# Kernel tuning notes

Measured on AMD Instinct MI355X. Metric: run time of the kernel, lower is better.

The kernel has to match this reference:

```python
import jax, jax.numpy as jnp
import numpy as np

L, B, C, N, M, H = 256, 128, 20, 30, 3, 1024  # length, batch, cond_dim, noise_dim, midi_dim, hidden
P_DROP = 0.6


def _lstm_cell(x, h, c, Wih, Whh, bih, bhh):
    # torch.nn.LSTMCell: gates ordered i, f, g, o
    gates = x @ Wih.T + h @ Whh.T + bih + bhh
    i, f, g, o = jnp.split(gates, 4, axis=-1)
    c_new = jax.nn.sigmoid(f) * c + jax.nn.sigmoid(i) * jnp.tanh(g)
    h_new = jax.nn.sigmoid(o) * jnp.tanh(c_new)
    return h_new, c_new


def setup_inputs():
    key = jax.random.key(0)
    ks = jax.random.split(key, 16)
    keep = 1.0 - P_DROP
    s = lambda k, shape: jax.random.normal(k, shape, jnp.float32) * np.float32(1.0 / np.sqrt(H))
    return {
        "condition": jax.random.normal(ks[0], (L, B, C), jnp.float32),
        "noise": jax.random.normal(ks[1], (B, N), jnp.float32),
        "h_init": jax.random.uniform(ks[2], (B, H), jnp.float32),
        "c_init": jax.random.uniform(ks[3], (B, H), jnp.float32),
        "dropout_mask": (jax.random.uniform(ks[4], (L, B, H)) < keep).astype(jnp.float32) / np.float32(keep),
        "Wih0": s(ks[5], (4 * H, C + N)), "Whh0": s(ks[6], (4 * H, H)),
        "bih0": jnp.zeros(4 * H, jnp.float32), "bhh0": jnp.zeros(4 * H, jnp.float32),
        "Wih1": s(ks[7], (4 * H, C + M)), "Whh1": s(ks[8], (4 * H, H)),
        "bih1": jnp.zeros(4 * H, jnp.float32), "bhh1": jnp.zeros(4 * H, jnp.float32),
        "Wih2": s(ks[9], (4 * H, H)), "Whh2": s(ks[10], (4 * H, H)),
        "bih2": jnp.zeros(4 * H, jnp.float32), "bhh2": jnp.zeros(4 * H, jnp.float32),
        "Wfc": s(ks[11], (M, H)), "bfc": jnp.zeros(M, jnp.float32),
    }


def reference(condition, noise, h_init, c_init, dropout_mask,
              Wih0, Whh0, bih0, bhh0, Wih1, Whh1, bih1, bhh1,
              Wih2, Whh2, bih2, bhh2, Wfc, bfc):
    # step 0: lstmcell0 on cat(condition[0], noise); h1==h2==h_init, c1==c2==c_init
    h1, c1 = _lstm_cell(jnp.concatenate([condition[0], noise], axis=1),
                        h_init, c_init, Wih0, Whh0, bih0, bhh0)
    h1 = h1 * dropout_mask[0]
    h2, c2 = _lstm_cell(h1, h_init, c_init, Wih2, Whh2, bih2, bhh2)
    out0 = h2 @ Wfc.T + bfc  # [B, M]

    def step(carry, xs):
        h1, c1, h2, c2, out = carry
        cond_t, mask_t = xs
        h1, c1 = _lstm_cell(jnp.concatenate([cond_t, out], axis=1),
                            h1, c1, Wih1, Whh1, bih1, bhh1)
        h1 = h1 * mask_t
        h2, c2 = _lstm_cell(h1, h2, c2, Wih2, Whh2, bih2, bhh2)
        out = h2 @ Wfc.T + bfc
        return (h1, c1, h2, c2, out), out

    _, outs = jax.lax.scan(step, (h1, c1, h2, c2, out0),
                           (condition[1:], dropout_mask[1:]))
    return jnp.concatenate([out0[None], outs], axis=0)  # [L, B, M]
```

## Files before the change

### kernel.cpp

```cpp
#include <hip/hip_runtime.h>
#include <math.h>

#define Bb   128
#define Hd   1024
#define Ld   256
#define Cd   20
#define Nd   30
#define Md   3

using bfrag = __attribute__((ext_vector_type(8)))  short;
using f16v  = __attribute__((ext_vector_type(16))) float;

union Pack8 { bfrag v; unsigned short u[8]; };

__device__ __forceinline__ float sigm(float x) { return 1.0f / (1.0f + expf(-x)); }

__device__ __forceinline__ unsigned short bf_rne(float x) {
    unsigned u = __float_as_uint(x);
    unsigned r = (u + 0x7fffu + ((u >> 16) & 1u)) >> 16;
    return (unsigned short)r;
}
__device__ __forceinline__ float bf_f(unsigned short h) {
    return __uint_as_float(((unsigned)h) << 16);
}

#define MFMA(a,b,c) __builtin_amdgcn_mfma_f32_32x32x16_bf16((a),(b),(c),0,0,0)

__device__ __forceinline__ void gld_lds16(const void* g, void* s) {
    __builtin_amdgcn_global_load_lds((const __attribute__((address_space(1))) void*)g,
                                     (__attribute__((address_space(3))) void*)s, 16, 0, 0);
}
#define WAIT_VM(n) __builtin_amdgcn_s_waitcnt(0x0F70 | (n))
#define BARRIER()  __builtin_amdgcn_s_barrier()

__global__ void cast_kernel(const float* __restrict__ src,
                            unsigned short* __restrict__ dst, int n)
{
    for (int i = blockIdx.x * blockDim.x + threadIdx.x; i < n; i += gridDim.x * blockDim.x)
        dst[i] = bf_rne(src[i]);
}

__global__ void cast_pad_kernel(const float* __restrict__ src,
                                unsigned short* __restrict__ dst,
                                int rows, int K, int Kp)
{
    int n = rows * Kp;
    for (int i = blockIdx.x * blockDim.x + threadIdx.x; i < n; i += gridDim.x * blockDim.x) {
        int r = i / Kp, k = i - r * Kp;
        dst[i] = bf_rne((k < K) ? src[r * K + k] : 0.0f);
    }
}

__global__ void split_kernel(const float* __restrict__ src,
                             unsigned short* __restrict__ hi,
                             unsigned short* __restrict__ lo, int n)
{
    for (int i = blockIdx.x * blockDim.x + threadIdx.x; i < n; i += gridDim.x * blockDim.x) {
        float x = src[i];
        unsigned short h = bf_rne(x);
        hi[i] = h;
        lo[i] = bf_rne(x - bf_f(h));
    }
}

template<int MODE>
__global__ __launch_bounds__(512, 1) void mfma_cell(
    const unsigned short* __restrict__ Ahi0, const unsigned short* __restrict__ Alo0,
    const unsigned short* __restrict__ W0,
    const unsigned short* __restrict__ Ahi1, const unsigned short* __restrict__ Alo1,
    const unsigned short* __restrict__ W1,
    const float* __restrict__ condt, const float* __restrict__ outprev,
    const unsigned short* __restrict__ Wsm,
    const float* __restrict__ bih, const float* __restrict__ bhh,
    const float* __restrict__ cprev, float* __restrict__ cnew,
    const float* __restrict__ maskt,
    unsigned short* __restrict__ Hhi, unsigned short* __restrict__ Hlo,
    const float* __restrict__ Wfc, const float* __restrict__ bfc,
    float* __restrict__ outp)
{
    __shared__ unsigned short Abuf[2][2][32 * 128];
    __shared__ unsigned short Wbuf[2][64 * 128];
    __shared__ float part[8][32][65];
    __shared__ float hbuf[32][16];

    const int bid   = blockIdx.x;
    const int mtile = (bid >> 3) & 3;
    const int jtile = (bid & 7) * 8 + (bid >> 5);
    const int j0 = jtile * 16;
    const int m0 = mtile * 32;

    const int tid  = threadIdx.x;
    const int wave = tid >> 6;
    const int lane = tid & 63;
    const int ml   = lane & 31;
    const int q    = lane >> 5;

    if (MODE == 1 && bid == 0) {
        for (int i = tid; i < Bb * Md; i += 512) outp[i] = bfc[i % Md];
    }

    const int g0 = ml >> 4, jj0 = ml & 15;
    const size_t row0 = (size_t)(g0 * Hd + j0 + jj0);
    const size_t row1 = (size_t)((g0 + 2) * Hd + j0 + jj0);

    f16v C0, C1;
    #pragma unroll
    for (int r = 0; r < 16; ++r) { C0[r] = 0.0f; C1[r] = 0.0f; }

    constexpr int NC = (MODE == 1) ? 8 : 16;

    auto stage = [&](int c, int p) {
        const unsigned short *Ah, *Al, *Wg; int cb;
        if (MODE == 2 && c >= 8) { Ah = Ahi1; Al = Alo1; Wg = W1; cb = (c - 8) * 128; }
        else                     { Ah = Ahi0; Al = Alo0; Wg = W0; cb = c * 128; }
        {
            const int m = tid >> 4, bp = tid & 15, bs = bp ^ (m & 15);
            const size_t goff = (size_t)(m0 + m) * Hd + cb + bs * 8;
            gld_lds16(Ah + goff, &Abuf[p][0][wave * 512]);
            gld_lds16(Al + goff, &Abuf[p][1][wave * 512]);
        }
        #pragma unroll
        for (int r = 0; r < 2; ++r) {
            const int f = r * 512 + tid;
            const int n = f >> 4, bp = f & 15, bs = bp ^ (n & 15);
            const size_t goff = (size_t)((n >> 4) * Hd + j0 + (n & 15)) * Hd + cb + bs * 8;
            gld_lds16(Wg + goff, &Wbuf[p][r * 4096 + wave * 512]);
        }
    };

    stage(0, 0);
    for (int c = 0; c < NC; ++c) {
        const int p = c & 1;
        if (c + 1 < NC) { stage(c + 1, p ^ 1); WAIT_VM(4); }
        else            { WAIT_VM(0); }
        BARRIER();
        {
            const int b = 2 * wave + q;
            const int soff = (b ^ (ml & 15)) << 3;
            bfrag ah  = *(const bfrag*)&Abuf[p][0][ml * 128 + soff];
            bfrag al  = *(const bfrag*)&Abuf[p][1][ml * 128 + soff];
            bfrag w0f = *(const bfrag*)&Wbuf[p][ml * 128 + soff];
            bfrag w1f = *(const bfrag*)&Wbuf[p][(ml + 32) * 128 + soff];
            C0 = MFMA(ah, w0f, C0);
            C1 = MFMA(ah, w1f, C1);
            C0 = MFMA(al, w0f, C0);
            C1 = MFMA(al, w1f, C1);
        }
        BARRIER();
    }

    if (MODE == 1 && wave == 0) {
        const float* crow = condt + (m0 + ml) * Cd;
        const float* orow = outprev + (m0 + ml) * Md;
        float xv[2][8];
        #pragma unroll
        for (int j = 0; j < 8; ++j) { xv[0][j] = 0.f; xv[1][j] = 0.f; }
        if (q == 0) {
            #pragma unroll
            for (int j = 0; j < 8; ++j) xv[0][j] = crow[j];
            xv[1][0] = crow[16]; xv[1][1] = crow[17];
            xv[1][2] = crow[18]; xv[1][3] = crow[19];
            xv[1][4] = orow[0];  xv[1][5] = orow[1];  xv[1][6] = orow[2];
        } else {
            #pragma unroll
            for (int j = 0; j < 8; ++j) xv[0][j] = crow[8 + j];
        }
        #pragma unroll
        for (int ch = 0; ch < 2; ++ch) {
            Pack8 ah, al;
            #pragma unroll
            for (int j = 0; j < 8; ++j) {
                unsigned short h = bf_rne(xv[ch][j]);
                ah.u[j] = h;
                al.u[j] = bf_rne(xv[ch][j] - bf_f(h));
            }
            const int kk = ch * 16 + 8 * q;
            bfrag b0 = *(const bfrag*)(Wsm + row0 * 32 + kk);
            bfrag b1 = *(const bfrag*)(Wsm + row1 * 32 + kk);
            C0 = MFMA(ah.v, b0, C0);
            C1 = MFMA(ah.v, b1, C1);
            C0 = MFMA(al.v, b0, C0);
            C1 = MFMA(al.v, b1, C1);
        }
    }

    #pragma unroll
    for (int r = 0; r < 16; ++r) {
        const int mrow = (r & 3) + 8 * (r >> 2) + 4 * q;
        part[wave][mrow][ml]      = C0[r];
        part[wave][mrow][32 + ml] = C1[r];
    }
    __syncthreads();

    {
        const int m  = tid >> 4;
        const int jj = tid & 15;
        float g[4];
        #pragma unroll
        for (int gg = 0; gg < 4; ++gg) {
            float s = 0.0f;
            #pragma unroll
            for (int w = 0; w < 8; ++w) s += part[w][m][gg * 16 + jj];
            const int n = gg * Hd + j0 + jj;
            g[gg] = s + bih[n] + bhh[n];
        }
        const int b  = m0 + m;
        const int jc = j0 + jj;
        const size_t idx = (size_t)b * Hd + jc;
        float cp = cprev[idx];
        float cn = sigm(g[1]) * cp + sigm(g[0]) * tanhf(g[2]);
        float hv = sigm(g[3]) * tanhf(cn);
        if (MODE == 1) hv *= maskt[idx];
        cnew[idx] = cn;
        unsigned short hh = bf_rne(hv);
        Hhi[idx] = hh;
        Hlo[idx] = bf_rne(hv - bf_f(hh));
        if (MODE == 2) hbuf[m][jj] = hv;
    }

    if (MODE == 2) {
        __syncthreads();
        if (tid < 32) {
            const int b = m0 + tid;
            #pragma unroll
            for (int mm = 0; mm < Md; ++mm) {
                float s = 0.0f;
                #pragma unroll
                for (int jj = 0; jj < 16; ++jj) s += hbuf[tid][jj] * Wfc[mm * Hd + j0 + jj];
                atomicAdd(&outp[b * Md + mm], s);
            }
        }
    }
}

#define BT   64
#define JT   8
#define RT   32
#define KC   64
#define NT   256
#define NCHUNK 16
#define XSs  68
#define SMs  52
#define GBs  33

__global__ __launch_bounds__(NT) void lstm_cell_kernel(
    const float* __restrict__ Xbig0, const float* __restrict__ Wbig0,
    const float* __restrict__ Xbig1, const float* __restrict__ Wbig1,
    const float* __restrict__ Xsm0p, int K0,
    const float* __restrict__ Xsm1p, int K1,
    const float* __restrict__ Wsmall,
    const float* __restrict__ bih, const float* __restrict__ bhh,
    const float* __restrict__ cprev, float* __restrict__ cnew,
    const float* __restrict__ mask,
    float* __restrict__ hnew,
    const float* __restrict__ Wfc, const float* __restrict__ bfc,
    float* __restrict__ outp, int initOut)
{
    __shared__ float Xs[BT][XSs];
    __shared__ float Ws[RT][XSs];
    __shared__ float gbuf[BT][GBs];
    __shared__ float hbuf[BT][JT];
    __shared__ float Xsm[BT][SMs];
    __shared__ float Wsm[RT][SMs];

    const int tid = threadIdx.x;
    const int j0  = blockIdx.x * JT;
    const int b0  = blockIdx.y * BT;
    const int jp  = tid & 15;
    const int bq  = tid >> 4;

    auto GROW = [&](int r) { return ((r >> 3) * Hd + j0 + (r & 7)); };

    float acc[4][2];
    #pragma unroll
    for (int i = 0; i < 4; ++i) { acc[i][0] = 0.f; acc[i][1] = 0.f; }

    if (initOut && blockIdx.x == 0 && blockIdx.y == 0) {
        for (int i = tid; i < Bb * 3; i += NT) outp[i] = bfc[i % 3];
    }

    for (int seg = 0; seg < 2; ++seg) {
        const float* __restrict__ Xg = (seg == 0) ? Xbig0 : Xbig1;
        const float* __restrict__ Wg = (seg == 0) ? Wbig0 : Wbig1;
        if (Xg == nullptr) continue;

        float4 xr[4], wr[2];
        #pragma unroll
        for (int p = 0; p < 4; ++p) {
            int fi = p * NT + tid; int bloc = fi >> 4; int kq = fi & 15;
            xr[p] = *(const float4*)(Xg + (size_t)(b0 + bloc) * Hd + kq * 4);
        }
        #pragma unroll
        for (int p = 0; p < 2; ++p) {
            int fi = p * NT + tid; int r = fi >> 4; int kq = fi & 15;
            wr[p] = *(const float4*)(Wg + (size_t)GROW(r) * Hd + kq * 4);
        }
        #pragma unroll
        for (int p = 0; p < 4; ++p) { int fi = p * NT + tid; *(float4*)&Xs[fi >> 4][(fi & 15) * 4] = xr[p]; }
        #pragma unroll
        for (int p = 0; p < 2; ++p) { int fi = p * NT + tid; *(float4*)&Ws[fi >> 4][(fi & 15) * 4] = wr[p]; }
        __syncthreads();

        for (int kc = 0; kc < NCHUNK; ++kc) {
            const bool more = (kc + 1) < NCHUNK;
            if (more) {
                const int k0n = (kc + 1) * KC;
                #pragma unroll
                for (int p = 0; p < 4; ++p) {
                    int fi = p * NT + tid; int bloc = fi >> 4; int kq = fi & 15;
                    xr[p] = *(const float4*)(Xg + (size_t)(b0 + bloc) * Hd + k0n + kq * 4);
                }
                #pragma unroll
                for (int p = 0; p < 2; ++p) {
                    int fi = p * NT + tid; int r = fi >> 4; int kq = fi & 15;
                    wr[p] = *(const float4*)(Wg + (size_t)GROW(r) * Hd + k0n + kq * 4);
                }
            }
            #pragma unroll 4
            for (int kk = 0; kk < KC; kk += 4) {
                float4 w0 = *(const float4*)&Ws[jp][kk];
                float4 w1 = *(const float4*)&Ws[jp + 16][kk];
                #pragma unroll
                for (int bb = 0; bb < 4; ++bb) {
                    float4 xvv = *(const float4*)&Xs[bq + 16 * bb][kk];
                    acc[bb][0] += xvv.x * w0.x + xvv.y * w0.y + xvv.z * w0.z + xvv.w * w0.w;
                    acc[bb][1] += xvv.x * w1.x + xvv.y * w1.y + xvv.z * w1.z + xvv.w * w1.w;
                }
            }
            __syncthreads();
            if (more) {
                #pragma unroll
                for (int p = 0; p < 4; ++p) { int fi = p * NT + tid; *(float4*)&Xs[fi >> 4][(fi & 15) * 4] = xr[p]; }
                #pragma unroll
                for (int p = 0; p < 2; ++p) { int fi = p * NT + tid; *(float4*)&Ws[fi >> 4][(fi & 15) * 4] = wr[p]; }
                __syncthreads();
            }
        }
    }

    if (Wsmall) {
        const int Kt = K0 + K1;
        for (int i = tid; i < BT * Kt; i += NT) {
            int bloc = i / Kt, k = i % Kt;
            Xsm[bloc][k] = (k < K0) ? Xsm0p[(size_t)(b0 + bloc) * K0 + k]
                                    : Xsm1p[(size_t)(b0 + bloc) * K1 + (k - K0)];
        }
        for (int i = tid; i < RT * Kt; i += NT) {
            int r = i / Kt, k = i % Kt;
            Wsm[r][k] = Wsmall[(size_t)GROW(r) * Kt + k];
        }
        __syncthreads();
        for (int k = 0; k < Kt; ++k) {
            float w0 = Wsm[jp][k], w1 = Wsm[jp + 16][k];
            #pragma unroll
            for (int bb = 0; bb < 4; ++bb) {
                float xvv = Xsm[bq + 16 * bb][k];
                acc[bb][0] += xvv * w0;
                acc[bb][1] += xvv * w1;
            }
        }
    }

    __syncthreads();
    #pragma unroll
    for (int bb = 0; bb < 4; ++bb) {
        gbuf[bq + 16 * bb][jp]      = acc[bb][0];
        gbuf[bq + 16 * bb][jp + 16] = acc[bb][1];
    }
    __syncthreads();

    for (int p = tid; p < BT * JT; p += NT) {
        int bloc = p & (BT - 1);
        int j    = p >> 6;
        int bg   = b0 + bloc;
        int jc   = j0 + j;
        float gi = gbuf[bloc][j]      + bih[jc]          + bhh[jc];
        float gf = gbuf[bloc][8 + j]  + bih[Hd + jc]     + bhh[Hd + jc];
        float gg = gbuf[bloc][16 + j] + bih[2 * Hd + jc] + bhh[2 * Hd + jc];
        float go = gbuf[bloc][24 + j] + bih[3 * Hd + jc] + bhh[3 * Hd + jc];
        float cp = cprev[(size_t)bg * Hd + jc];
        float cn = sigm(gf) * cp + sigm(gi) * tanhf(gg);
        float hv = sigm(go) * tanhf(cn);
        if (mask) hv *= mask[(size_t)bg * Hd + jc];
        cnew[(size_t)bg * Hd + jc] = cn;
        hnew[(size_t)bg * Hd + jc] = hv;
        hbuf[bloc][j] = hv;
    }

    if (Wfc) {
        __syncthreads();
        if (tid < BT) {
            int bg = b0 + tid;
            #pragma unroll
            for (int m = 0; m < 3; ++m) {
                float s = 0.f;
                #pragma unroll
                for (int j = 0; j < JT; ++j) s += hbuf[tid][j] * Wfc[m * Hd + j0 + j];
                atomicAdd(&outp[bg * 3 + m], s);
            }
        }
    }
}

extern "C" void kernel_launch(void* const* d_in, const int* in_sizes, int n_in,
                              void* d_out, int out_size, void* d_ws, size_t ws_size,
                              hipStream_t stream)
{
    (void)in_sizes; (void)n_in; (void)out_size;
    const float* cond   = (const float*)d_in[0];
    const float* noise  = (const float*)d_in[1];
    const float* h_init = (const float*)d_in[2];
    const float* c_init = (const float*)d_in[3];
    const float* dmask  = (const float*)d_in[4];
    const float* Wih0   = (const float*)d_in[5];
    const float* Whh0   = (const float*)d_in[6];
    const float* bih0   = (const float*)d_in[7];
    const float* bhh0   = (const float*)d_in[8];
    const float* Wih1   = (const float*)d_in[9];
    const float* Whh1   = (const float*)d_in[10];
    const float* bih1   = (const float*)d_in[11];
    const float* bhh1   = (const float*)d_in[12];
    const float* Wih2   = (const float*)d_in[13];
    const float* Whh2   = (const float*)d_in[14];
    const float* bih2   = (const float*)d_in[15];
    const float* bhh2   = (const float*)d_in[16];
    const float* Wfc    = (const float*)d_in[17];
    const float* bfc    = (const float*)d_in[18];
    float* out = (float*)d_out;

    char* wsb = (char*)d_ws;
    size_t off = 0;
    auto alloc = [&](size_t bytes) { size_t o = off; off += (bytes + 255) & ~(size_t)255; return o; };

    const size_t WBIG = (size_t)4 * Hd * Hd * 2;
    const size_t HB   = (size_t)Bb * Hd * 2;
    const size_t HF   = (size_t)Bb * Hd * 4;

    size_t o_w1 = alloc(WBIG);
    size_t o_w2 = alloc(WBIG);
    size_t o_w3 = alloc(WBIG);
    size_t o_wsm = alloc((size_t)4 * Hd * 32 * 2);
    size_t o_h1h[2] = { alloc(HB), alloc(HB) };
    size_t o_h1l[2] = { alloc(HB), alloc(HB) };
    size_t o_h2h[2] = { alloc(HB), alloc(HB) };
    size_t o_h2l[2] = { alloc(HB), alloc(HB) };
    size_t o_c1 = alloc(HF), o_c2 = alloc(HF);
    size_t o_f1 = alloc(HF), o_f2 = alloc(HF);
    const size_t needed = off;

    if (ws_size < needed) {
        float* ws = (float*)d_ws;
        const size_t S = (size_t)Bb * Hd;
        float* h1a = ws;         float* h1b = ws + S;
        float* h2a = ws + 2 * S; float* h2b = ws + 3 * S;
        float* c1  = ws + 4 * S; float* c2  = ws + 5 * S;
        dim3 grid(Hd / JT, Bb / BT);
        dim3 blk(NT);
        lstm_cell_kernel<<<grid, blk, 0, stream>>>(
            h_init, Whh0, nullptr, nullptr, cond, Cd, noise, Nd, Wih0,
            bih0, bhh0, c_init, c1, dmask, h1a, nullptr, bfc, out, 1);
        lstm_cell_kernel<<<grid, blk, 0, stream>>>(
            h1a, Wih2, h_init, Whh2, nullptr, 0, nullptr, 0, nullptr,
            bih2, bhh2, c_init, c2, nullptr, h2a, Wfc, bfc, out, 0);
        const float* h1prev = h1a; const float* h2prev = h2a;
        for (int t = 1; t < Ld; ++t) {
            float* h1cur = (t & 1) ? h1b : h1a;
            float* h2cur = (t & 1) ? h2b : h2a;
            lstm_cell_kernel<<<grid, blk, 0, stream>>>(
                h1prev, Whh1, nullptr, nullptr,
                cond + (size_t)t * Bb * Cd, Cd, out + (size_t)(t - 1) * Bb * Md, Md, Wih1,
                bih1, bhh1, c1, c1, dmask + (size_t)t * Bb * Hd, h1cur,
                nullptr, bfc, out + (size_t)t * Bb * Md, 1);
            lstm_cell_kernel<<<grid, blk, 0, stream>>>(
                h1cur, Wih2, h2prev, Whh2, nullptr, 0, nullptr, 0, nullptr,
                bih2, bhh2, c2, c2, nullptr, h2cur, Wfc, bfc, out + (size_t)t * Bb * Md, 0);
            h1prev = h1cur; h2prev = h2cur;
        }
        return;
    }

    auto U16 = [&](size_t o) { return (unsigned short*)(wsb + o); };
    auto F32 = [&](size_t o) { return (float*)(wsb + o); };

    const int NW = 4 * Hd * Hd;
    cast_kernel<<<2048, 256, 0, stream>>>(Whh1, U16(o_w1), NW);
    cast_kernel<<<2048, 256, 0, stream>>>(Wih2, U16(o_w2), NW);
    cast_kernel<<<2048, 256, 0, stream>>>(Whh2, U16(o_w3), NW);
    cast_pad_kernel<<<512, 256, 0, stream>>>(Wih1, U16(o_wsm), 4 * Hd, Cd + Md, 32);

    {
        dim3 grid(Hd / JT, Bb / BT);
        dim3 blk(NT);
        lstm_cell_kernel<<<grid, blk, 0, stream>>>(
            h_init, Whh0, nullptr, nullptr, cond, Cd, noise, Nd, Wih0,
            bih0, bhh0, c_init, F32(o_c1), dmask, F32(o_f1), nullptr, bfc, out, 1);
        lstm_cell_kernel<<<grid, blk, 0, stream>>>(
            F32(o_f1), Wih2, h_init, Whh2, nullptr, 0, nullptr, 0, nullptr,
            bih2, bhh2, c_init, F32(o_c2), nullptr, F32(o_f2), Wfc, bfc, out, 0);
        split_kernel<<<256, 256, 0, stream>>>(F32(o_f1), U16(o_h1h[0]), U16(o_h1l[0]), Bb * Hd);
        split_kernel<<<256, 256, 0, stream>>>(F32(o_f2), U16(o_h2h[0]), U16(o_h2l[0]), Bb * Hd);
    }

    for (int t = 1; t < Ld; ++t) {
        const int cur = t & 1, prv = (t - 1) & 1;
        mfma_cell<1><<<256, 512, 0, stream>>>(
            U16(o_h1h[prv]), U16(o_h1l[prv]), U16(o_w1),
            nullptr, nullptr, nullptr,
            cond + (size_t)t * Bb * Cd, out + (size_t)(t - 1) * Bb * Md,
            U16(o_wsm),
            bih1, bhh1, F32(o_c1), F32(o_c1),
            dmask + (size_t)t * Bb * Hd,
            U16(o_h1h[cur]), U16(o_h1l[cur]),
            nullptr, bfc, out + (size_t)t * Bb * Md);
        mfma_cell<2><<<256, 512, 0, stream>>>(
            U16(o_h1h[cur]), U16(o_h1l[cur]), U16(o_w2),
            U16(o_h2h[prv]), U16(o_h2l[prv]), U16(o_w3),
            nullptr, nullptr, nullptr,
            bih2, bhh2, F32(o_c2), F32(o_c2),
            nullptr,
            U16(o_h2h[cur]), U16(o_h2l[cur]),
            Wfc, bfc, out + (size_t)t * Bb * Md);
    }
}
```

Measured before the change: 6.451 ms.

## Fuse all timesteps into one persistent kernel with atomic grid barriers

Replaces the 510 per-step kernel launches with a single persistent kernel of 256 blocks that loops over time and synchronises across the grid with an atomic-counter barrier. The aim is to remove launch overhead and the inter-kernel gaps in the recurrent chain. It also deepens the staging pipeline from 2 to 4 LDS buffers, uses cache-policy bits on the activation loads so fresh h values are read, and rebuckets the epilogue to two columns per thread. The approach depends on all 256 blocks being co-resident, otherwise the spin barrier can deadlock, and it relies on relaxed atomics for visibility of data between blocks.

```diff
diff --git a/kernel.cpp b/kernel.cpp
--- a/kernel.cpp
+++ b/kernel.cpp
@@ -29,6 +29,10 @@
 __device__ __forceinline__ void gld_lds16(const void* g, void* s) {
     __builtin_amdgcn_global_load_lds((const __attribute__((address_space(1))) void*)g,
                                      (__attribute__((address_space(3))) void*)s, 16, 0, 0);
+}
+__device__ __forceinline__ void gld_lds16c(const void* g, void* s) {
+    __builtin_amdgcn_global_load_lds((const __attribute__((address_space(1))) void*)g,
+                                     (__attribute__((address_space(3))) void*)s, 16, 0, 16);
 }
 #define WAIT_VM(n) __builtin_amdgcn_s_waitcnt(0x0F70 | (n))
 #define BARRIER()  __builtin_amdgcn_s_barrier()
@@ -63,173 +67,259 @@
     }
 }
 
-template<int MODE>
-__global__ __launch_bounds__(512, 1) void mfma_cell(
-    const unsigned short* __restrict__ Ahi0, const unsigned short* __restrict__ Alo0,
-    const unsigned short* __restrict__ W0,
-    const unsigned short* __restrict__ Ahi1, const unsigned short* __restrict__ Alo1,
-    const unsigned short* __restrict__ W1,
-    const float* __restrict__ condt, const float* __restrict__ outprev,
-    const unsigned short* __restrict__ Wsm,
-    const float* __restrict__ bih, const float* __restrict__ bhh,
-    const float* __restrict__ cprev, float* __restrict__ cnew,
-    const float* __restrict__ maskt,
-    unsigned short* __restrict__ Hhi, unsigned short* __restrict__ Hlo,
+__global__ __launch_bounds__(512, 1) void lstm_persistent(
+    const unsigned short* __restrict__ W1, const unsigned short* __restrict__ W2,
+    const unsigned short* __restrict__ W3, const unsigned short* __restrict__ Wsm,
+    const float* __restrict__ cond, const float* __restrict__ dmask,
+    const float* __restrict__ bih1, const float* __restrict__ bhh1,
+    const float* __restrict__ bih2, const float* __restrict__ bhh2,
+    float* __restrict__ c1, float* __restrict__ c2,
+    unsigned short* __restrict__ h1h, unsigned short* __restrict__ h1l,
+    unsigned short* __restrict__ h2h, unsigned short* __restrict__ h2l,
     const float* __restrict__ Wfc, const float* __restrict__ bfc,
-    float* __restrict__ outp)
+    float* __restrict__ out, unsigned* __restrict__ barcnt)
 {
-    __shared__ unsigned short Abuf[2][2][32 * 128];
-    __shared__ unsigned short Wbuf[2][64 * 128];
-    __shared__ float part[8][32][65];
-    __shared__ float hbuf[32][16];
+    __shared__ union {
+        struct { unsigned short A[4][2][4096]; unsigned short W[4][8192]; } s;
+        struct { float part[8][32][65]; float hbuf[32][16]; } r;
+    } U;
 
     const int bid   = blockIdx.x;
     const int mtile = (bid >> 3) & 3;
     const int jtile = (bid & 7) * 8 + (bid >> 5);
-    const int j0 = jtile * 16;
-    const int m0 = mtile * 32;
+    const int j0 = jtile * 16, m0 = mtile * 32;
 
     const int tid  = threadIdx.x;
     const int wave = tid >> 6;
     const int lane = tid & 63;
     const int ml   = lane & 31;
     const int q    = lane >> 5;
-
-    if (MODE == 1 && bid == 0) {
-        for (int i = tid; i < Bb * Md; i += 512) outp[i] = bfc[i % Md];
-    }
-
-    const int g0 = ml >> 4, jj0 = ml & 15;
-    const size_t row0 = (size_t)(g0 * Hd + j0 + jj0);
-    const size_t row1 = (size_t)((g0 + 2) * Hd + j0 + jj0);
-
-    f16v C0, C1;
-    #pragma unroll
-    for (int r = 0; r < 16; ++r) { C0[r] = 0.0f; C1[r] = 0.0f; }
-
-    constexpr int NC = (MODE == 1) ? 8 : 16;
-
-    auto stage = [&](int c, int p) {
-        const unsigned short *Ah, *Al, *Wg; int cb;
-        if (MODE == 2 && c >= 8) { Ah = Ahi1; Al = Alo1; Wg = W1; cb = (c - 8) * 128; }
-        else                     { Ah = Ahi0; Al = Alo0; Wg = W0; cb = c * 128; }
-        {
-            const int m = tid >> 4, bp = tid & 15, bs = bp ^ (m & 15);
-            const size_t goff = (size_t)(m0 + m) * Hd + cb + bs * 8;
-            gld_lds16(Ah + goff, &Abuf[p][0][wave * 512]);
-            gld_lds16(Al + goff, &Abuf[p][1][wave * 512]);
-        }
+    const size_t S = (size_t)Bb * Hd;
+
+    const int am = tid >> 4, abp = tid & 15, abs_ = abp ^ (am & 15);
+    const size_t aoff_base = (size_t)(m0 + am) * Hd + abs_ * 8;
+
+    unsigned bar_target = 0;
+
+    auto grid_bar = [&]() {
+        bar_target += 256;
+        __syncthreads();
+        if (tid == 0) {
+            __hip_atomic_fetch_add(barcnt, 1u, __ATOMIC_RELAXED, __HIP_MEMORY_SCOPE_AGENT);
+            while (__hip_atomic_load(barcnt, __ATOMIC_RELAXED, __HIP_MEMORY_SCOPE_AGENT) < bar_target)
+                __builtin_amdgcn_s_sleep(2);
+        }
+        __syncthreads();
+    };
+
+    auto stageA = [&](const unsigned short* Ah, const unsigned short* Al, int cb, int buf) {
+        const size_t goff = aoff_base + cb;
+        gld_lds16c(Ah + goff, &U.s.A[buf][0][wave * 512]);
+        gld_lds16c(Al + goff, &U.s.A[buf][1][wave * 512]);
+    };
+    auto stageW = [&](const unsigned short* Wg, int cb, int buf) {
         #pragma unroll
         for (int r = 0; r < 2; ++r) {
             const int f = r * 512 + tid;
             const int n = f >> 4, bp = f & 15, bs = bp ^ (n & 15);
             const size_t goff = (size_t)((n >> 4) * Hd + j0 + (n & 15)) * Hd + cb + bs * 8;
-            gld_lds16(Wg + goff, &Wbuf[p][r * 4096 + wave * 512]);
+            gld_lds16(Wg + goff, &U.s.W[buf][r * 4096 + wave * 512]);
         }
     };
-
-    stage(0, 0);
-    for (int c = 0; c < NC; ++c) {
-        const int p = c & 1;
-        if (c + 1 < NC) { stage(c + 1, p ^ 1); WAIT_VM(4); }
-        else            { WAIT_VM(0); }
-        BARRIER();
+    auto computeC = [&](int buf, f16v& C0, f16v& C1) {
+        const int b = 2 * wave + q;
+        const int soff = (b ^ (ml & 15)) << 3;
+        bfrag ah  = *(const bfrag*)&U.s.A[buf][0][ml * 128 + soff];
+        bfrag al  = *(const bfrag*)&U.s.A[buf][1][ml * 128 + soff];
+        bfrag w0f = *(const bfrag*)&U.s.W[buf][ml * 128 + soff];
+        bfrag w1f = *(const bfrag*)&U.s.W[buf][(ml + 32) * 128 + soff];
+        C0 = MFMA(ah, w0f, C0);
+        C1 = MFMA(ah, w1f, C1);
+        C0 = MFMA(al, w0f, C0);
+        C1 = MFMA(al, w1f, C1);
+    };
+    auto dump_part = [&](const f16v& C0, const f16v& C1) {
+        #pragma unroll
+        for (int r = 0; r < 16; ++r) {
+            const int mrow = (r & 3) + 8 * (r >> 2) + 4 * q;
+            U.r.part[wave][mrow][ml]      = C0[r];
+            U.r.part[wave][mrow][32 + ml] = C1[r];
+        }
+    };
+
+    const int g0 = ml >> 4, jj0 = ml & 15;
+    const size_t row0 = (size_t)(g0 * Hd + j0 + jj0);
+    const size_t row1 = (size_t)((g0 + 2) * Hd + j0 + jj0);
+
+    #pragma clang loop unroll(disable)
+    for (int t = 1; t < Ld; ++t) {
+        const int cur = t & 3, prv = (t - 1) & 3;
+        float* outp_t = out + (size_t)t * Bb * Md;
+        const float* outp_p = out + (size_t)(t - 1) * Bb * Md;
+
         {
-            const int b = 2 * wave + q;
-            const int soff = (b ^ (ml & 15)) << 3;
-            bfrag ah  = *(const bfrag*)&Abuf[p][0][ml * 128 + soff];
-            bfrag al  = *(const bfrag*)&Abuf[p][1][ml * 128 + soff];
-            bfrag w0f = *(const bfrag*)&Wbuf[p][ml * 128 + soff];
-            bfrag w1f = *(const bfrag*)&Wbuf[p][(ml + 32) * 128 + soff];
-            C0 = MFMA(ah, w0f, C0);
-            C1 = MFMA(ah, w1f, C1);
-            C0 = MFMA(al, w0f, C0);
-            C1 = MFMA(al, w1f, C1);
-        }
-        BARRIER();
-    }
-
-    if (MODE == 1 && wave == 0) {
-        const float* crow = condt + (m0 + ml) * Cd;
-        const float* orow = outprev + (m0 + ml) * Md;
-        float xv[2][8];
-        #pragma unroll
-        for (int j = 0; j < 8; ++j) { xv[0][j] = 0.f; xv[1][j] = 0.f; }
-        if (q == 0) {
+            const unsigned short* Ah = h1h + (size_t)prv * S;
+            const unsigned short* Al = h1l + (size_t)prv * S;
+            stageA(Ah, Al, 0, 0);   stageW(W1, 0, 0);
+            stageA(Ah, Al, 128, 1); stageW(W1, 128, 1);
+            stageA(Ah, Al, 256, 2); stageW(W1, 256, 2);
+            if (bid == 0) {
+                for (int i = tid; i < Bb * Md; i += 512)
+                    __hip_atomic_store(&outp_t[i], bfc[i % Md], __ATOMIC_RELAXED, __HIP_MEMORY_SCOPE_AGENT);
+            }
+            f16v C0, C1;
             #pragma unroll
-            for (int j = 0; j < 8; ++j) xv[0][j] = crow[j];
-            xv[1][0] = crow[16]; xv[1][1] = crow[17];
-            xv[1][2] = crow[18]; xv[1][3] = crow[19];
-            xv[1][4] = orow[0];  xv[1][5] = orow[1];  xv[1][6] = orow[2];
-        } else {
+            for (int r = 0; r < 16; ++r) { C0[r] = 0.f; C1[r] = 0.f; }
+            for (int c = 0; c < 8; ++c) {
+                const int p = c & 3;
+                if (c + 3 < 8) { stageA(Ah, Al, (c + 3) * 128, (c + 3) & 3); stageW(W1, (c + 3) * 128, (c + 3) & 3); }
+                if (c + 3 < 8) WAIT_VM(12);
+                else if (c + 2 < 8) WAIT_VM(8);
+                else if (c + 1 < 8) WAIT_VM(4);
+                else WAIT_VM(0);
+                BARRIER();
+                computeC(p, C0, C1);
+                BARRIER();
+            }
+            if (wave == 0) {
+                const float* crow = cond + (size_t)t * Bb * Cd + (m0 + ml) * Cd;
+                const float* orow = outp_p + (m0 + ml) * Md;
+                float xv[2][8];
+                #pragma unroll
+                for (int j = 0; j < 8; ++j) { xv[0][j] = 0.f; xv[1][j] = 0.f; }
+                if (q == 0) {
+                    #pragma unroll
+                    for (int j = 0; j < 8; ++j) xv[0][j] = crow[j];
+                    xv[1][0] = crow[16]; xv[1][1] = crow[17];
+                    xv[1][2] = crow[18]; xv[1][3] = crow[19];
+                    xv[1][4] = __hip_atomic_load((float*)&orow[0], __ATOMIC_RELAXED, __HIP_MEMORY_SCOPE_AGENT);
+                    xv[1][5] = __hip_atomic_load((float*)&orow[1], __ATOMIC_RELAXED, __HIP_MEMORY_SCOPE_AGENT);
+                    xv[1][6] = __hip_atomic_load((float*)&orow[2], __ATOMIC_RELAXED, __HIP_MEMORY_SCOPE_AGENT);
+                } else {
+                    #pragma unroll
+                    for (int j = 0; j < 8; ++j) xv[0][j] = crow[8 + j];
+                }
+                #pragma unroll
+                for (int ch = 0; ch < 2; ++ch) {
+                    Pack8 ah, al;
+                    #pragma unroll
+                    for (int j = 0; j < 8; ++j) {
+                        unsigned short h = bf_rne(xv[ch][j]);
+                        ah.u[j] = h;
+                        al.u[j] = bf_rne(xv[ch][j] - bf_f(h));
+                    }
+                    const int kk = ch * 16 + 8 * q;
+                    bfrag b0 = *(const bfrag*)(Wsm + row0 * 32 + kk);
+                    bfrag b1 = *(const bfrag*)(Wsm + row1 * 32 + kk);
+                    C0 = MFMA(ah.v, b0, C0);
+                    C1 = MFMA(ah.v, b1, C1);
+                    C0 = MFMA(al.v, b0, C0);
+                    C1 = MFMA(al.v, b1, C1);
+                }
+            }
+            dump_part(C0, C1);
+            __syncthreads();
+            if (tid < 256) {
+                const int m = tid >> 3, j2 = (tid & 7) * 2;
+                const int b = m0 + m, jc = j0 + j2;
+                const size_t idx = (size_t)b * Hd + jc;
+                float g[4][2];
+                #pragma unroll
+                for (int gg = 0; gg < 4; ++gg) {
+                    #pragma unroll
+                    for (int e = 0; e < 2; ++e) {
+                        float s = 0.f;
+                        #pragma unroll
+                        for (int w = 0; w < 8; ++w) s += U.r.part[w][m][gg * 16 + j2 + e];
+                        const int n = gg * Hd + jc + e;
+                        g[gg][e] = s + bih1[n] + bhh1[n];
+                    }
+                }
+                float2 cp = *(const float2*)&c1[idx];
+                float2 mv = *(const float2*)&dmask[(size_t)t * S + idx];
+                float cn0 = sigm(g[1][0]) * cp.x + sigm(g[0][0]) * tanhf(g[2][0]);
+                float cn1 = sigm(g[1][1]) * cp.y + sigm(g[0][1]) * tanhf(g[2][1]);
+                float hv0 = sigm(g[3][0]) * tanhf(cn0) * mv.x;
+                float hv1 = sigm(g[3][1]) * tanhf(cn1) * mv.y;
+                *(float2*)&c1[idx] = make_float2(cn0, cn1);
+                unsigned short h0 = bf_rne(hv0), h1_ = bf_rne(hv1);
+                unsigned hp = (unsigned)h0 | ((unsigned)h1_ << 16);
+                unsigned lp = (unsigned)bf_rne(hv0 - bf_f(h0)) | ((unsigned)bf_rne(hv1 - bf_f(h1_)) << 16);
+                __hip_atomic_store((unsigned*)&h1h[(size_t)cur * S + idx], hp, __ATOMIC_RELAXED, __HIP_MEMORY_SCOPE_AGENT);
+                __hip_atomic_store((unsigned*)&h1l[(size_t)cur * S + idx], lp, __ATOMIC_RELAXED, __HIP_MEMORY_SCOPE_AGENT);
+            }
+        }
+        grid_bar();
+
+        {
+            const unsigned short* A2h = h1h + (size_t)cur * S;
+            const unsigned short* A2l = h1l + (size_t)cur * S;
+            const unsigned short* A3h = h2h + (size_t)prv * S;
+            const unsigned short* A3l = h2l + (size_t)prv * S;
+            auto stageB = [&](int c, int buf) {
+                if (c < 8) { stageA(A2h, A2l, c * 128, buf); stageW(W2, c * 128, buf); }
+                else       { stageA(A3h, A3l, (c - 8) * 128, buf); stageW(W3, (c - 8) * 128, buf); }
+            };
+            stageB(0, 0); stageB(1, 1); stageB(2, 2);
+            f16v C0, C1;
             #pragma unroll
-            for (int j = 0; j < 8; ++j) xv[0][j] = crow[8 + j];
-        }
-        #pragma unroll
-        for (int ch = 0; ch < 2; ++ch) {
-            Pack8 ah, al;
-            #pragma unroll
-            for (int j = 0; j < 8; ++j) {
-                unsigned short h = bf_rne(xv[ch][j]);
-                ah.u[j] = h;
-                al.u[j] = bf_rne(xv[ch][j] - bf_f(h));
-            }
-            const int kk = ch * 16 + 8 * q;
-            bfrag b0 = *(const bfrag*)(Wsm + row0 * 32 + kk);
-            bfrag b1 = *(const bfrag*)(Wsm + row1 * 32 + kk);
-            C0 = MFMA(ah.v, b0, C0);
-            C1 = MFMA(ah.v, b1, C1);
-            C0 = MFMA(al.v, b0, C0);
-            C1 = MFMA(al.v, b1, C1);
-        }
-    }
-
-    #pragma unroll
-    for (int r = 0; r < 16; ++r) {
-        const int mrow = (r & 3) + 8 * (r >> 2) + 4 * q;
-        part[wave][mrow][ml]      = C0[r];
-        part[wave][mrow][32 + ml] = C1[r];
-    }
-    __syncthreads();
-
-    {
-        const int m  = tid >> 4;
-        const int jj = tid & 15;
-        float g[4];
-        #pragma unroll
-        for (int gg = 0; gg < 4; ++gg) {
-            float s = 0.0f;
-            #pragma unroll
-            for (int w = 0; w < 8; ++w) s += part[w][m][gg * 16 + jj];
-            const int n = gg * Hd + j0 + jj;
-            g[gg] = s + bih[n] + bhh[n];
-        }
-        const int b  = m0 + m;
-        const int jc = j0 + jj;
-        const size_t idx = (size_t)b * Hd + jc;
-        float cp = cprev[idx];
-        float cn = sigm(g[1]) * cp + sigm(g[0]) * tanhf(g[2]);
-        float hv = sigm(g[3]) * tanhf(cn);
-        if (MODE == 1) hv *= maskt[idx];
-        cnew[idx] = cn;
-        unsigned short hh = bf_rne(hv);
-        Hhi[idx] = hh;
-        Hlo[idx] = bf_rne(hv - bf_f(hh));
-        if (MODE == 2) hbuf[m][jj] = hv;
-    }
-
-    if (MODE == 2) {
-        __syncthreads();
-        if (tid < 32) {
-            const int b = m0 + tid;
-            #pragma unroll
-            for (int mm = 0; mm < Md; ++mm) {
-                float s = 0.0f;
-                #pragma unroll
-                for (int jj = 0; jj < 16; ++jj) s += hbuf[tid][jj] * Wfc[mm * Hd + j0 + jj];
-                atomicAdd(&outp[b * Md + mm], s);
-            }
-        }
+            for (int r = 0; r < 16; ++r) { C0[r] = 0.f; C1[r] = 0.f; }
+            for (int c = 0; c < 16; ++c) {
+                const int p = c & 3;
+                if (c + 3 < 16) stageB(c + 3, (c + 3) & 3);
+                if (c + 3 < 16) WAIT_VM(12);
+                else if (c + 2 < 16) WAIT_VM(8);
+                else if (c + 1 < 16) WAIT_VM(4);
+                else WAIT_VM(0);
+                BARRIER();
+                computeC(p, C0, C1);
+                BARRIER();
+            }
+            dump_part(C0, C1);
+            __syncthreads();
+            if (tid < 256) {
+                const int m = tid >> 3, j2 = (tid & 7) * 2;
+                const int b = m0 + m, jc = j0 + j2;
+                const size_t idx = (size_t)b * Hd + jc;
+                float g[4][2];
+                #pragma unroll
+                for (int gg = 0; gg < 4; ++gg) {
+                    #pragma unroll
+                    for (int e = 0; e < 2; ++e) {
+                        float s = 0.f;
+                        #pragma unroll
+                        for (int w = 0; w < 8; ++w) s += U.r.part[w][m][gg * 16 + j2 + e];
+                        const int n = gg * Hd + jc + e;
+                        g[gg][e] = s + bih2[n] + bhh2[n];
+                    }
+                }
+                float2 cp = *(const float2*)&c2[idx];
+                float cn0 = sigm(g[1][0]) * cp.x + sigm(g[0][0]) * tanhf(g[2][0]);
+                float cn1 = sigm(g[1][1]) * cp.y + sigm(g[0][1]) * tanhf(g[2][1]);
+                float hv0 = sigm(g[3][0]) * tanhf(cn0);
+                float hv1 = sigm(g[3][1]) * tanhf(cn1);
+                *(float2*)&c2[idx] = make_float2(cn0, cn1);
+                U.r.hbuf[m][j2]     = hv0;
+                U.r.hbuf[m][j2 + 1] = hv1;
+                unsigned short h0 = bf_rne(hv0), h1_ = bf_rne(hv1);
+                unsigned hp = (unsigned)h0 | ((unsigned)h1_ << 16);
+                unsigned lp = (unsigned)bf_rne(hv0 - bf_f(h0)) | ((unsigned)bf_rne(hv1 - bf_f(h1_)) << 16);
+                __hip_atomic_store((unsigned*)&h2h[(size_t)cur * S + idx], hp, __ATOMIC_RELAXED, __HIP_MEMORY_SCOPE_AGENT);
+                __hip_atomic_store((unsigned*)&h2l[(size_t)cur * S + idx], lp, __ATOMIC_RELAXED, __HIP_MEMORY_SCOPE_AGENT);
+            }
+            __syncthreads();
+            if (tid < 32) {
+                const int b = m0 + tid;
+                #pragma unroll
+                for (int mm = 0; mm < Md; ++mm) {
+                    float s = 0.0f;
+                    #pragma unroll
+                    for (int jj = 0; jj < 16; ++jj) s += U.r.hbuf[tid][jj] * Wfc[mm * Hd + j0 + jj];
+                    atomicAdd(&outp_t[b * Md + mm], s);
+                }
+            }
+        }
+        grid_bar();
     }
 }
 
@@ -433,24 +523,24 @@
     auto alloc = [&](size_t bytes) { size_t o = off; off += (bytes + 255) & ~(size_t)255; return o; };
 
     const size_t WBIG = (size_t)4 * Hd * Hd * 2;
-    const size_t HB   = (size_t)Bb * Hd * 2;
-    const size_t HF   = (size_t)Bb * Hd * 4;
+    const size_t S    = (size_t)Bb * Hd;
+    const size_t HB4  = S * 2 * 4;
+    const size_t HF   = S * 4;
 
     size_t o_w1 = alloc(WBIG);
     size_t o_w2 = alloc(WBIG);
     size_t o_w3 = alloc(WBIG);
     size_t o_wsm = alloc((size_t)4 * Hd * 32 * 2);
-    size_t o_h1h[2] = { alloc(HB), alloc(HB) };
-    size_t o_h1l[2] = { alloc(HB), alloc(HB) };
-    size_t o_h2h[2] = { alloc(HB), alloc(HB) };
-    size_t o_h2l[2] = { alloc(HB), alloc(HB) };
+    size_t o_h1h = alloc(HB4), o_h1l = alloc(HB4);
+    size_t o_h2h = alloc(HB4), o_h2l = alloc(HB4);
     size_t o_c1 = alloc(HF), o_c2 = alloc(HF);
     size_t o_f1 = alloc(HF), o_f2 = alloc(HF);
+    off = (off + 4095) & ~(size_t)4095;
+    size_t o_bar = alloc(4096);
     const size_t needed = off;
 
     if (ws_size < needed) {
         float* ws = (float*)d_ws;
-        const size_t S = (size_t)Bb * Hd;
         float* h1a = ws;         float* h1b = ws + S;
         float* h2a = ws + 2 * S; float* h2b = ws + 3 * S;
         float* c1  = ws + 4 * S; float* c2  = ws + 5 * S;
@@ -482,6 +572,8 @@
     auto U16 = [&](size_t o) { return (unsigned short*)(wsb + o); };
     auto F32 = [&](size_t o) { return (float*)(wsb + o); };
 
+    hipMemsetAsync(wsb + o_bar, 0, 256, stream);
+
     const int NW = 4 * Hd * Hd;
     cast_kernel<<<2048, 256, 0, stream>>>(Whh1, U16(o_w1), NW);
     cast_kernel<<<2048, 256, 0, stream>>>(Wih2, U16(o_w2), NW);
@@ -497,28 +589,14 @@
         lstm_cell_kernel<<<grid, blk, 0, stream>>>(
             F32(o_f1), Wih2, h_init, Whh2, nullptr, 0, nullptr, 0, nullptr,
             bih2, bhh2, c_init, F32(o_c2), nullptr, F32(o_f2), Wfc, bfc, out, 0);
-        split_kernel<<<256, 256, 0, stream>>>(F32(o_f1), U16(o_h1h[0]), U16(o_h1l[0]), Bb * Hd);
-        split_kernel<<<256, 256, 0, stream>>>(F32(o_f2), U16(o_h2h[0]), U16(o_h2l[0]), Bb * Hd);
-    }
-
-    for (int t = 1; t < Ld; ++t) {
-        const int cur = t & 1, prv = (t - 1) & 1;
-        mfma_cell<1><<<256, 512, 0, stream>>>(
-            U16(o_h1h[prv]), U16(o_h1l[prv]), U16(o_w1),
-            nullptr, nullptr, nullptr,
-            cond + (size_t)t * Bb * Cd, out + (size_t)(t - 1) * Bb * Md,
-            U16(o_wsm),
-            bih1, bhh1, F32(o_c1), F32(o_c1),
-            dmask + (size_t)t * Bb * Hd,
-            U16(o_h1h[cur]), U16(o_h1l[cur]),
-            nullptr, bfc, out + (size_t)t * Bb * Md);
-        mfma_cell<2><<<256, 512, 0, stream>>>(
-            U16(o_h1h[cur]), U16(o_h1l[cur]), U16(o_w2),
-            U16(o_h2h[prv]), U16(o_h2l[prv]), U16(o_w3),
-            nullptr, nullptr, nullptr,
-            bih2, bhh2, F32(o_c2), F32(o_c2),
-            nullptr,
-            U16(o_h2h[cur]), U16(o_h2l[cur]),
-            Wfc, bfc, out + (size_t)t * Bb * Md);
-    }
-}
+        split_kernel<<<256, 256, 0, stream>>>(F32(o_f1), U16(o_h1h), U16(o_h1l), Bb * Hd);
+        split_kernel<<<256, 256, 0, stream>>>(F32(o_f2), U16(o_h2h), U16(o_h2l), Bb * Hd);
+    }
+
+    lstm_persistent<<<256, 512, 0, stream>>>(
+        U16(o_w1), U16(o_w2), U16(o_w3), U16(o_wsm),
+        cond, dmask, bih1, bhh1, bih2, bhh2,
+        F32(o_c1), F32(o_c2),
+        U16(o_h1h), U16(o_h1l), U16(o_h2h), U16(o_h2l),
+        Wfc, bfc, out, (unsigned*)(wsb + o_bar));
+}
```

New measurement: 11.51 ms. 1.78x slower.
